# Kernel tuning notes

Hardware: AMD Instinct MI355X
Metric: run time of the kernel (lower is better)

Reference implementation:

```python
import jax, jax.numpy as jnp
import numpy as np

KEYS = ["A1", "B2", "E1", "E2", "E3", "E4", "E5"]
DIMS = [1, 1, 2, 2, 2, 2, 2]  # irrep dimensions for D12 point group
H = 8  # num_heads


def setup_inputs() -> dict:
    key = jax.random.key(0)
    ks = jax.random.split(key, 11)
    B, S, M = 8, 1024, 64  # batch, seq_len, multiplicity per key
    inp = {}
    for i, (name, d) in enumerate(zip(KEYS, DIMS)):
        inp[f"x_{name}"] = jax.random.normal(ks[i], (B, S, d, M), dtype=jnp.float32)
    for j, wn in enumerate(["Wq", "Wk", "Wv", "Wo"]):
        # per-key nn.Linear weights [out_mult, in_mult], stacked over the 7 keys
        inp[wn] = jax.random.normal(ks[7 + j], (7, M, M), dtype=jnp.float32) / np.float32(np.sqrt(M))
    return inp


def _split_heads(v):
    # [B,S,d,m] -> [B,H,S,d*mk]
    B, S, d, m = v.shape
    mk = m // H
    return v.reshape(B, S, d, H, mk).transpose(0, 3, 1, 2, 4).reshape(B, H, S, d * mk)


def _combine_heads(v, d):
    # [B,H,S,d*mk] -> [B,S,d,H*mk]
    B, _, S, dmk = v.shape
    mk = dmk // d
    return v.reshape(B, H, S, d, mk).transpose(0, 2, 3, 1, 4).reshape(B, S, d, H * mk)


def _forward(xs, Wq, Wk, Wv, Wo):
    # per-key bias-free linears on the multiplicity (last) axis; nn.Linear does x @ W.T
    qs = [_split_heads(jnp.einsum('bsdi,oi->bsdo', x, Wq[i])) for i, x in enumerate(xs)]
    kks = [_split_heads(jnp.einsum('bsdi,oi->bsdo', x, Wk[i])) for i, x in enumerate(xs)]
    vs = [_split_heads(jnp.einsum('bsdi,oi->bsdo', x, Wv[i])) for i, x in enumerate(xs)]
    Q = jnp.concatenate(qs, axis=-1)  # [B,H,S,D], D = sum d_k*mk = 96
    K = jnp.concatenate(kks, axis=-1)
    scale = np.float32(1.0 / np.sqrt(Q.shape[-1]))
    probs = jax.nn.softmax(jnp.einsum('bhqd,bhkd->bhqk', Q, K) * scale, axis=-1)
    outs = []
    for i, (v, d) in enumerate(zip(vs, DIMS)):
        o = jnp.einsum('bhqk,bhkd->bhqd', probs, v)  # shared softmax over per-key V branches
        o = _combine_heads(o, d)  # [B,S,d,M]
        outs.append(jnp.einsum('bsdi,oi->bsdo', o, Wo[i]))
    # concatenate the 7 per-key outputs along the irrep-dimension axis: [B,S,12,M]
    return jnp.concatenate(outs, axis=2)


def reference(x_A1, x_B2, x_E1, x_E2, x_E3, x_E4, x_E5, Wq, Wk, Wv, Wo):
    xs = [x_A1, x_B2, x_E1, x_E2, x_E3, x_E4, x_E5]
    return _forward(xs, Wq, Wk, Wv, Wo)
```

## Files before the change

### kernel.cpp

```cpp
#include <hip/hip_runtime.h>
#include <stdint.h>

typedef __attribute__((ext_vector_type(8))) short bf16x8;
typedef __attribute__((ext_vector_type(4))) float f32x4;
typedef unsigned short ushort_t;

__device__ __forceinline__ unsigned short f2bf(float f){
  union { float f; unsigned u; } c; c.f = f;
  unsigned u = c.u;
  u = u + 0x7FFFu + ((u >> 16) & 1u);
  return (unsigned short)(u >> 16);
}

__device__ __forceinline__ bf16x8 cvt8(const float* p){
  const float4 a = ((const float4*)p)[0];
  const float4 b = ((const float4*)p)[1];
  bf16x8 r;
  r[0]=(short)f2bf(a.x); r[1]=(short)f2bf(a.y); r[2]=(short)f2bf(a.z); r[3]=(short)f2bf(a.w);
  r[4]=(short)f2bf(b.x); r[5]=(short)f2bf(b.y); r[6]=(short)f2bf(b.z); r[7]=(short)f2bf(b.w);
  return r;
}

__device__ __forceinline__ uint32_t pk2bf(float a, float b){
  uint32_t r;
  asm("v_cvt_pk_bf16_f32 %0, %1, %2" : "=v"(r) : "v"(a), "v"(b));
  return r;
}

__device__ __forceinline__ float exp2x(float x){
  float r;
  asm("v_exp_f32 %0, %1" : "=v"(r) : "v"(x));
  return r;
}

__device__ __forceinline__ void gll16(const ushort_t* g, short* l){
  __builtin_amdgcn_global_load_lds(
      (const __attribute__((address_space(1))) unsigned int*)g,
      (__attribute__((address_space(3))) unsigned int*)l, 16, 0, 0);
}

__global__ __launch_bounds__(256) void wconv(
    const float* __restrict__ Wq, const float* __restrict__ Wk,
    const float* __restrict__ Wv, const float* __restrict__ Wo,
    ushort_t* __restrict__ out)
{
  const int a = blockIdx.y;
  const float* src = (a==0)?Wq:(a==1)?Wk:(a==2)?Wv:Wo;
  const float sc = (a==0) ? 0.14724743479535623f : 1.0f;
  const int i = (blockIdx.x*256 + threadIdx.x)*8;
  float4 v0 = *(const float4*)(src+i);
  float4 v1 = *(const float4*)(src+i+4);
  uint4 o;
  o.x = pk2bf(v0.x*sc, v0.y*sc);
  o.y = pk2bf(v0.z*sc, v0.w*sc);
  o.z = pk2bf(v1.x*sc, v1.y*sc);
  o.w = pk2bf(v1.z*sc, v1.w*sc);
  *(uint4*)(out + (size_t)a*28672 + i) = o;
}

__global__ __launch_bounds__(256) void qkv_proj(
    const float* __restrict__ xA1, const float* __restrict__ xB2,
    const float* __restrict__ xE1, const float* __restrict__ xE2,
    const float* __restrict__ xE3, const float* __restrict__ xE4,
    const float* __restrict__ xE5,
    const ushort_t* __restrict__ Wb4,
    ushort_t* __restrict__ Qg, ushort_t* __restrict__ Kg,
    ushort_t* __restrict__ Vg)
{
  const int dims[7] = {1,1,2,2,2,2,2};
  const int rrb_[7] = {0,1,2,4,6,8,10};
  const int tile = blockIdx.x;
  int i = 0, t0 = 0;
  for (int k = 0; k < 7; ++k){
    int n = 128 * dims[k];
    if (tile >= t0 + n) t0 += n; else { i = k; break; }
  }
  const int d = dims[i], rrb = rrb_[i];
  const float* xp = (i==0)?xA1:(i==1)?xB2:(i==2)?xE1:(i==3)?xE2:(i==4)?xE3:(i==5)?xE4:xE5;

  const int lane = threadIdx.x & 63;
  const int w    = threadIdx.x >> 6;
  const int lo = lane & 15, hi = lane >> 4;
  const int row0 = (tile - t0) * 64 + w * 16;

  bf16x8 afr[2];
  {
    const float* rp = xp + (size_t)(row0 + lo) * 64;
    afr[0] = cvt8(rp + 8*hi);
    afr[1] = cvt8(rp + 32 + 8*hi);
  }

  ushort_t* Ob[3] = {Qg, Kg, Vg};

  #pragma unroll
  for (int wsel = 0; wsel < 3; ++wsel){
    const ushort_t* Wb = Wb4 + (size_t)wsel*28672 + (size_t)i * 64 * 64;
    #pragma unroll
    for (int ot = 0; ot < 4; ++ot){
      f32x4 acc = {0.f,0.f,0.f,0.f};
      #pragma unroll
      for (int c = 0; c < 2; ++c){
        bf16x8 bfr = *(const bf16x8*)(Wb + (size_t)(lo + 16*ot) * 64 + 32*c + 8*hi);
        acc = __builtin_amdgcn_mfma_f32_16x16x32_bf16(afr[c], bfr, acc, 0, 0, 0);
      }
      const int o  = lo + 16*ot;
      const int hh = o >> 3, mm = o & 7;
      #pragma unroll
      for (int r = 0; r < 4; ++r){
        int R  = row0 + hi*4 + r;
        int bs = (d == 2) ? (R >> 1) : R;
        int dx = (d == 2) ? (R & 1)  : 0;
        int bb = bs >> 10, s = bs & 1023;
        int rr = rrb + dx;
        size_t tb = (size_t)((bb*8 + hh)*16 + (s >> 6)) * 6144;
        unsigned short val = f2bf(acc[r]);
        if (wsel < 2){
          size_t a = tb + (size_t)(((((s>>4)&3)*3 + (rr>>2))*64 + (rr&3)*16 + (s&15)))*8 + mm;
          Ob[wsel][a] = val;
        } else {
          int s6 = s & 63, rem = s6 & 31;
          int jj = (rem & 3) + ((rem >> 4) << 2);
          int f  = rr*8 + mm;
          size_t a = tb + (size_t)((((s6>>5)*6 + (f>>4))*64 + ((rem>>2)&3)*16 + (f&15)))*8 + jj;
          Ob[2][a] = val;
        }
      }
    }
  }
}

__global__ __launch_bounds__(256, 2) void attn(
    const ushort_t* __restrict__ Qg,
    const ushort_t* __restrict__ Kg,
    const ushort_t* __restrict__ Vg,
    ushort_t* __restrict__ Oc)
{
  __shared__ __align__(16) short Kl[2][6144];
  __shared__ __align__(16) short Vl[2][6144];

  const int bid = blockIdx.x;
  const int bh = (bid & 7)*8 + ((bid >> 3) & 7);
  const int qt = bid >> 6;
  const int b = bh >> 3, h = bh & 7;
  const int tid = threadIdx.x;
  const int w = tid >> 6, lane = tid & 63;
  const int lo = lane & 15, hi = lane >> 4;
  const size_t base = (size_t)bh * 16 * 6144;

  bf16x8 qf[2][3];
  #pragma unroll
  for (int g = 0; g < 2; ++g){
    int qq = qt*128 + w*32 + g*16;
    const ushort_t* qb = Qg + base + (size_t)(qq >> 6)*6144 + (size_t)(((qq>>4)&3)*3)*512;
    #pragma unroll
    for (int c = 0; c < 3; ++c)
      qf[g][c] = *(const bf16x8*)(qb + (c*64 + lane)*8);
  }

  f32x4 acc[6][2];
  #pragma unroll
  for (int ft = 0; ft < 6; ++ft){ acc[ft][0] = (f32x4){0,0,0,0}; acc[ft][1] = (f32x4){0,0,0,0}; }
  float mr[2] = {-1e30f, -1e30f}, lr[2] = {0.f, 0.f};

#define STAGE(tt, bb) do { \
    const ushort_t* kg_ = Kg + base + (size_t)(tt)*6144 + tid*8; \
    const ushort_t* vg_ = Vg + base + (size_t)(tt)*6144 + tid*8; \
    short* kl_ = &Kl[bb][tid*8]; short* vl_ = &Vl[bb][tid*8]; \
    gll16(kg_,        kl_);        gll16(kg_ + 2048, kl_ + 2048); \
    gll16(kg_ + 4096, kl_ + 4096); gll16(vg_,        vl_); \
    gll16(vg_ + 2048, vl_ + 2048); gll16(vg_ + 4096, vl_ + 4096); \
  } while(0)

  STAGE(0, 0);
  __syncthreads();

  for (int t = 0; t < 16; ++t){
    if (t < 15) STAGE(t+1, (t+1)&1);
    const int cb = t & 1;

    f32x4 st[2][4];
    #pragma unroll
    for (int kvb = 0; kvb < 4; ++kvb){
      bf16x8 kf[3];
      #pragma unroll
      for (int c = 0; c < 3; ++c)
        kf[c] = *(const bf16x8*)&Kl[cb][((kvb*3 + c)*64 + lane)*8];
      #pragma unroll
      for (int g = 0; g < 2; ++g){
        f32x4 s = {0.f,0.f,0.f,0.f};
        #pragma unroll
        for (int c = 0; c < 3; ++c)
          s = __builtin_amdgcn_mfma_f32_16x16x32_bf16(kf[c], qf[g][c], s, 0, 0, 0);
        st[g][kvb] = s;
      }
    }

    bf16x8 pb[2][2];
    #pragma unroll
    for (int g = 0; g < 2; ++g){
      float tm = st[g][0][0];
      #pragma unroll
      for (int kvb = 0; kvb < 4; ++kvb)
        #pragma unroll
        for (int r = 0; r < 4; ++r) tm = fmaxf(tm, st[g][kvb][r]);
      tm = fmaxf(tm, __shfl_xor(tm, 16));
      tm = fmaxf(tm, __shfl_xor(tm, 32));
      if (!__all(tm - mr[g] <= 8.f)){
        float mn = fmaxf(mr[g], tm);
        float al = exp2x(mr[g] - mn);
        lr[g] *= al;
        #pragma unroll
        for (int ft = 0; ft < 6; ++ft)
          #pragma unroll
          for (int r = 0; r < 4; ++r) acc[ft][g][r] *= al;
        mr[g] = mn;
      }
      float ps = 0.f;
      #pragma unroll
      for (int kvb = 0; kvb < 4; ++kvb)
        #pragma unroll
        for (int r = 0; r < 4; ++r){ st[g][kvb][r] = exp2x(st[g][kvb][r] - mr[g]); ps += st[g][kvb][r]; }
      ps += __shfl_xor(ps, 16);
      ps += __shfl_xor(ps, 32);
      lr[g] += ps;
      #pragma unroll
      for (int ch = 0; ch < 2; ++ch){
        union { uint32_t u[4]; bf16x8 v; } pu;
        pu.u[0] = pk2bf(st[g][2*ch  ][0], st[g][2*ch  ][1]);
        pu.u[1] = pk2bf(st[g][2*ch  ][2], st[g][2*ch  ][3]);
        pu.u[2] = pk2bf(st[g][2*ch+1][0], st[g][2*ch+1][1]);
        pu.u[3] = pk2bf(st[g][2*ch+1][2], st[g][2*ch+1][3]);
        pb[g][ch] = pu.v;
      }
    }

    #pragma unroll
    for (int ch = 0; ch < 2; ++ch){
      #pragma unroll
      for (int ft = 0; ft < 6; ++ft){
        bf16x8 va = *(const bf16x8*)&Vl[cb][((ch*6 + ft)*64 + lane)*8];
        acc[ft][0] = __builtin_amdgcn_mfma_f32_16x16x32_bf16(va, pb[0][ch], acc[ft][0], 0, 0, 0);
        acc[ft][1] = __builtin_amdgcn_mfma_f32_16x16x32_bf16(va, pb[1][ch], acc[ft][1], 0, 0, 0);
      }
    }

    __syncthreads();
  }
#undef STAGE

  #pragma unroll
  for (int g = 0; g < 2; ++g){
    float rl = 1.f / lr[g];
    int q = qt*128 + w*32 + g*16 + lo;
    #pragma unroll
    for (int ft = 0; ft < 6; ++ft){
      uint2 o;
      o.x = pk2bf(acc[ft][g][0]*rl, acc[ft][g][1]*rl);
      o.y = pk2bf(acc[ft][g][2]*rl, acc[ft][g][3]*rl);
      int f0 = ft*16 + 4*hi;
      int rr = f0 >> 3, mm0 = f0 & 7;
      size_t ad = ((size_t)(b*1024 + q)*12 + rr)*64 + h*8 + mm0;
      *(uint2*)(Oc + ad) = o;
    }
  }
}

__global__ __launch_bounds__(256) void out_proj(
    const ushort_t* __restrict__ Oc,
    const ushort_t* __restrict__ Wb4,
    float* __restrict__ out)
{
  const int dims[7] = {1,1,2,2,2,2,2};
  const int rrb_[7] = {0,1,2,4,6,8,10};
  const int tile = blockIdx.x;
  int i = 0, t0 = 0;
  for (int k = 0; k < 7; ++k){
    int n = 128 * dims[k];
    if (tile >= t0 + n) t0 += n; else { i = k; break; }
  }
  const int d = dims[i], rrb = rrb_[i];
  const int w = threadIdx.x >> 6, lane = threadIdx.x & 63;
  const int lo = lane & 15, hi = lane >> 4;
  const int row0 = (tile - t0) * 64 + w * 16;

  bf16x8 afr[2];
  {
    int R  = row0 + lo;
    int bs = (d == 2) ? (R >> 1) : R;
    int dx = (d == 2) ? (R & 1)  : 0;
    const ushort_t* rp = Oc + (size_t)(bs*12 + rrb + dx) * 64;
    afr[0] = *(const bf16x8*)(rp + 8*hi);
    afr[1] = *(const bf16x8*)(rp + 32 + 8*hi);
  }
  const ushort_t* Wb = Wb4 + (size_t)3*28672 + (size_t)i * 64 * 64;
  #pragma unroll
  for (int ot = 0; ot < 4; ++ot){
    f32x4 acc = {0.f,0.f,0.f,0.f};
    #pragma unroll
    for (int c = 0; c < 2; ++c){
      bf16x8 bfr = *(const bf16x8*)(Wb + (size_t)(lo + 16*ot) * 64 + 32*c + 8*hi);
      acc = __builtin_amdgcn_mfma_f32_16x16x32_bf16(afr[c], bfr, acc, 0, 0, 0);
    }
    #pragma unroll
    for (int r = 0; r < 4; ++r){
      int R  = row0 + hi*4 + r;
      int bs = (d == 2) ? (R >> 1) : R;
      int dx = (d == 2) ? (R & 1)  : 0;
      out[(size_t)(bs*12 + rrb + dx) * 64 + lo + 16*ot] = acc[r];
    }
  }
}

extern "C" void kernel_launch(void* const* d_in, const int* in_sizes, int n_in,
                              void* d_out, int out_size, void* d_ws, size_t ws_size,
                              hipStream_t stream)
{
  const float* xA1 = (const float*)d_in[0];
  const float* xB2 = (const float*)d_in[1];
  const float* xE1 = (const float*)d_in[2];
  const float* xE2 = (const float*)d_in[3];
  const float* xE3 = (const float*)d_in[4];
  const float* xE4 = (const float*)d_in[5];
  const float* xE5 = (const float*)d_in[6];
  const float* Wq  = (const float*)d_in[7];
  const float* Wk  = (const float*)d_in[8];
  const float* Wv  = (const float*)d_in[9];
  const float* Wo  = (const float*)d_in[10];

  const size_t NE = (size_t)8 * 1024 * 12 * 64;
  ushort_t* Qg = (ushort_t*)d_ws;
  ushort_t* Kg = Qg + NE;
  ushort_t* Vg = Kg + NE;
  ushort_t* Oc = Vg + NE;
  ushort_t* Wb4 = Oc + NE;

  wconv<<<dim3(14,4), dim3(256), 0, stream>>>(Wq, Wk, Wv, Wo, Wb4);
  qkv_proj<<<dim3(1536), dim3(256), 0, stream>>>(xA1,xB2,xE1,xE2,xE3,xE4,xE5,
                                                 Wb4, Qg,Kg,Vg);
  attn<<<dim3(512), dim3(256), 0, stream>>>(Qg,Kg,Vg, Oc);
  out_proj<<<dim3(1536), dim3(256), 0, stream>>>(Oc, Wb4, (float*)d_out);
}
```

Measured before the change: 81.95 us.

## Stage QKV stores through LDS, halve attention query tile, relayout Oc

qkv_proj now tiles by irrep row and writes each tile into shared memory first, then stores it to Q/K/V in 16-byte vectors instead of scattered 2-byte writes. The attention kernel handles 64 queries per block instead of 128 and launches twice as many blocks with a launch-bounds occupancy of 3. It also adds s_setprio around its MFMA phases. The attention output buffer gets a new head-major layout that out_proj reads with vector loads. The trade-off is more K/V reloads per query across blocks and extra LDS traffic plus barriers in the projection kernel.

```diff
diff --git a/kernel.cpp b/kernel.cpp
--- a/kernel.cpp
+++ b/kernel.cpp
@@ -37,6 +37,11 @@
   __builtin_amdgcn_global_load_lds(
       (const __attribute__((address_space(1))) unsigned int*)g,
       (__attribute__((address_space(3))) unsigned int*)l, 16, 0, 0);
+}
+
+__device__ __forceinline__ void rr_decode(int rr, int& i, int& dx, int& d){
+  if (rr < 2){ i = rr; dx = 0; d = 1; }
+  else { i = 2 + ((rr-2)>>1); dx = (rr-2)&1; d = 2; }
 }
 
 __global__ __launch_bounds__(256) void wconv(
@@ -67,25 +72,23 @@
     ushort_t* __restrict__ Qg, ushort_t* __restrict__ Kg,
     ushort_t* __restrict__ Vg)
 {
-  const int dims[7] = {1,1,2,2,2,2,2};
-  const int rrb_[7] = {0,1,2,4,6,8,10};
+  __shared__ short Cl[64*72];
+
   const int tile = blockIdx.x;
-  int i = 0, t0 = 0;
-  for (int k = 0; k < 7; ++k){
-    int n = 128 * dims[k];
-    if (tile >= t0 + n) t0 += n; else { i = k; break; }
-  }
-  const int d = dims[i], rrb = rrb_[i];
+  const int rr = tile >> 7, rt = tile & 127;
+  int i, dx, d; rr_decode(rr, i, dx, d);
   const float* xp = (i==0)?xA1:(i==1)?xB2:(i==2)?xE1:(i==3)?xE2:(i==4)?xE3:(i==5)?xE4:xE5;
 
   const int lane = threadIdx.x & 63;
   const int w    = threadIdx.x >> 6;
   const int lo = lane & 15, hi = lane >> 4;
-  const int row0 = (tile - t0) * 64 + w * 16;
+  const int b8 = (rt >> 4) * 8;
+  const int tile64 = rt & 15;
 
   bf16x8 afr[2];
   {
-    const float* rp = xp + (size_t)(row0 + lo) * 64;
+    const int R = rt*64 + w*16 + lo;
+    const float* rp = xp + (size_t)(R*d + dx) * 64;
     afr[0] = cvt8(rp + 8*hi);
     afr[1] = cvt8(rp + 32 + 8*hi);
   }
@@ -94,7 +97,7 @@
 
   #pragma unroll
   for (int wsel = 0; wsel < 3; ++wsel){
-    const ushort_t* Wb = Wb4 + (size_t)wsel*28672 + (size_t)i * 64 * 64;
+    const ushort_t* Wb = Wb4 + (size_t)wsel*28672 + (size_t)i * 4096;
     #pragma unroll
     for (int ot = 0; ot < 4; ++ot){
       f32x4 acc = {0.f,0.f,0.f,0.f};
@@ -103,33 +106,45 @@
         bf16x8 bfr = *(const bf16x8*)(Wb + (size_t)(lo + 16*ot) * 64 + 32*c + 8*hi);
         acc = __builtin_amdgcn_mfma_f32_16x16x32_bf16(afr[c], bfr, acc, 0, 0, 0);
       }
-      const int o  = lo + 16*ot;
-      const int hh = o >> 3, mm = o & 7;
-      #pragma unroll
-      for (int r = 0; r < 4; ++r){
-        int R  = row0 + hi*4 + r;
-        int bs = (d == 2) ? (R >> 1) : R;
-        int dx = (d == 2) ? (R & 1)  : 0;
-        int bb = bs >> 10, s = bs & 1023;
-        int rr = rrb + dx;
-        size_t tb = (size_t)((bb*8 + hh)*16 + (s >> 6)) * 6144;
-        unsigned short val = f2bf(acc[r]);
-        if (wsel < 2){
-          size_t a = tb + (size_t)(((((s>>4)&3)*3 + (rr>>2))*64 + (rr&3)*16 + (s&15)))*8 + mm;
-          Ob[wsel][a] = val;
-        } else {
-          int s6 = s & 63, rem = s6 & 31;
-          int jj = (rem & 3) + ((rem >> 4) << 2);
-          int f  = rr*8 + mm;
-          size_t a = tb + (size_t)((((s6>>5)*6 + (f>>4))*64 + ((rem>>2)&3)*16 + (f&15)))*8 + jj;
-          Ob[2][a] = val;
+      #pragma unroll
+      for (int r = 0; r < 4; ++r)
+        Cl[(w*16 + hi*4 + r)*72 + lo + 16*ot] = (short)f2bf(acc[r]);
+    }
+    __syncthreads();
+
+    if (wsel < 2){
+      #pragma unroll
+      for (int cc = 0; cc < 2; ++cc){
+        int c2 = threadIdx.x + cc*256;
+        int sl = c2 & 63, hh = c2 >> 6;
+        bf16x8 v = *(const bf16x8*)&Cl[sl*72 + hh*8];
+        size_t a = (size_t)((b8 + hh)*16 + tile64)*6144
+                 + (size_t)(((sl>>4)*3 + (rr>>2))*64 + (rr&3)*16 + (sl&15))*8;
+        *(bf16x8*)(Ob[wsel] + a) = v;
+      }
+    } else {
+      #pragma unroll
+      for (int cc = 0; cc < 2; ++cc){
+        int c2 = threadIdx.x + cc*256;
+        int mm = c2 & 7, hh = (c2>>3)&7, sblk = c2>>6;
+        int a5 = sblk>>2, slot = sblk&3;
+        short tmp[8];
+        #pragma unroll
+        for (int jj = 0; jj < 8; ++jj){
+          int s_j = a5*32 + (jj>>2)*16 + slot*4 + (jj&3);
+          tmp[jj] = Cl[s_j*72 + hh*8 + mm];
         }
-      }
-    }
-  }
-}
-
-__global__ __launch_bounds__(256, 2) void attn(
+        int fh = rr>>1, fl = (rr&1)*8 + mm;
+        size_t a = (size_t)((b8 + hh)*16 + tile64)*6144
+                 + (size_t)((a5*6 + fh)*64 + slot*16 + fl)*8;
+        *(bf16x8*)(Vg + a) = *(const bf16x8*)tmp;
+      }
+    }
+    __syncthreads();
+  }
+}
+
+__global__ __launch_bounds__(256, 3) void attn(
     const ushort_t* __restrict__ Qg,
     const ushort_t* __restrict__ Kg,
     const ushort_t* __restrict__ Vg,
@@ -141,26 +156,23 @@
   const int bid = blockIdx.x;
   const int bh = (bid & 7)*8 + ((bid >> 3) & 7);
   const int qt = bid >> 6;
-  const int b = bh >> 3, h = bh & 7;
   const int tid = threadIdx.x;
   const int w = tid >> 6, lane = tid & 63;
   const int lo = lane & 15, hi = lane >> 4;
   const size_t base = (size_t)bh * 16 * 6144;
 
-  bf16x8 qf[2][3];
+  bf16x8 qf[3];
+  {
+    const ushort_t* qb = Qg + base + (size_t)qt*6144 + (size_t)(w*3)*512;
+    #pragma unroll
+    for (int c = 0; c < 3; ++c)
+      qf[c] = *(const bf16x8*)(qb + (c*64 + lane)*8);
+  }
+
+  f32x4 acc[6];
   #pragma unroll
-  for (int g = 0; g < 2; ++g){
-    int qq = qt*128 + w*32 + g*16;
-    const ushort_t* qb = Qg + base + (size_t)(qq >> 6)*6144 + (size_t)(((qq>>4)&3)*3)*512;
-    #pragma unroll
-    for (int c = 0; c < 3; ++c)
-      qf[g][c] = *(const bf16x8*)(qb + (c*64 + lane)*8);
-  }
-
-  f32x4 acc[6][2];
-  #pragma unroll
-  for (int ft = 0; ft < 6; ++ft){ acc[ft][0] = (f32x4){0,0,0,0}; acc[ft][1] = (f32x4){0,0,0,0}; }
-  float mr[2] = {-1e30f, -1e30f}, lr[2] = {0.f, 0.f};
+  for (int ft = 0; ft < 6; ++ft) acc[ft] = (f32x4){0,0,0,0};
+  float mr = -1e30f, lr = 0.f;
 
 #define STAGE(tt, bb) do { \
     const ushort_t* kg_ = Kg + base + (size_t)(tt)*6144 + tid*8; \
@@ -178,88 +190,81 @@
     if (t < 15) STAGE(t+1, (t+1)&1);
     const int cb = t & 1;
 
-    f32x4 st[2][4];
+    f32x4 st[4];
+    __builtin_amdgcn_s_setprio(1);
     #pragma unroll
     for (int kvb = 0; kvb < 4; ++kvb){
-      bf16x8 kf[3];
-      #pragma unroll
-      for (int c = 0; c < 3; ++c)
-        kf[c] = *(const bf16x8*)&Kl[cb][((kvb*3 + c)*64 + lane)*8];
-      #pragma unroll
-      for (int g = 0; g < 2; ++g){
-        f32x4 s = {0.f,0.f,0.f,0.f};
+      f32x4 s = {0.f,0.f,0.f,0.f};
+      #pragma unroll
+      for (int c = 0; c < 3; ++c){
+        bf16x8 kf = *(const bf16x8*)&Kl[cb][((kvb*3 + c)*64 + lane)*8];
+        s = __builtin_amdgcn_mfma_f32_16x16x32_bf16(kf, qf[c], s, 0, 0, 0);
+      }
+      st[kvb] = s;
+    }
+    __builtin_amdgcn_s_setprio(0);
+
+    float tm = st[0][0];
+    #pragma unroll
+    for (int kvb = 0; kvb < 4; ++kvb)
+      #pragma unroll
+      for (int r = 0; r < 4; ++r) tm = fmaxf(tm, st[kvb][r]);
+    tm = fmaxf(tm, __shfl_xor(tm, 16));
+    tm = fmaxf(tm, __shfl_xor(tm, 32));
+    if (!__all(tm - mr <= 8.f)){
+      float mn = fmaxf(mr, tm);
+      float al = exp2x(mr - mn);
+      lr *= al;
+      #pragma unroll
+      for (int ft = 0; ft < 6; ++ft)
         #pragma unroll
-        for (int c = 0; c < 3; ++c)
-          s = __builtin_amdgcn_mfma_f32_16x16x32_bf16(kf[c], qf[g][c], s, 0, 0, 0);
-        st[g][kvb] = s;
-      }
-    }
-
-    bf16x8 pb[2][2];
-    #pragma unroll
-    for (int g = 0; g < 2; ++g){
-      float tm = st[g][0][0];
-      #pragma unroll
-      for (int kvb = 0; kvb < 4; ++kvb)
-        #pragma unroll
-        for (int r = 0; r < 4; ++r) tm = fmaxf(tm, st[g][kvb][r]);
-      tm = fmaxf(tm, __shfl_xor(tm, 16));
-      tm = fmaxf(tm, __shfl_xor(tm, 32));
-      if (!__all(tm - mr[g] <= 8.f)){
-        float mn = fmaxf(mr[g], tm);
-        float al = exp2x(mr[g] - mn);
-        lr[g] *= al;
-        #pragma unroll
-        for (int ft = 0; ft < 6; ++ft)
-          #pragma unroll
-          for (int r = 0; r < 4; ++r) acc[ft][g][r] *= al;
-        mr[g] = mn;
-      }
-      float ps = 0.f;
-      #pragma unroll
-      for (int kvb = 0; kvb < 4; ++kvb)
-        #pragma unroll
-        for (int r = 0; r < 4; ++r){ st[g][kvb][r] = exp2x(st[g][kvb][r] - mr[g]); ps += st[g][kvb][r]; }
-      ps += __shfl_xor(ps, 16);
-      ps += __shfl_xor(ps, 32);
-      lr[g] += ps;
-      #pragma unroll
-      for (int ch = 0; ch < 2; ++ch){
-        union { uint32_t u[4]; bf16x8 v; } pu;
-        pu.u[0] = pk2bf(st[g][2*ch  ][0], st[g][2*ch  ][1]);
-        pu.u[1] = pk2bf(st[g][2*ch  ][2], st[g][2*ch  ][3]);
-        pu.u[2] = pk2bf(st[g][2*ch+1][0], st[g][2*ch+1][1]);
-        pu.u[3] = pk2bf(st[g][2*ch+1][2], st[g][2*ch+1][3]);
-        pb[g][ch] = pu.v;
-      }
-    }
-
+        for (int r = 0; r < 4; ++r) acc[ft][r] *= al;
+      mr = mn;
+    }
+    float ps = 0.f;
+    #pragma unroll
+    for (int kvb = 0; kvb < 4; ++kvb)
+      #pragma unroll
+      for (int r = 0; r < 4; ++r){ st[kvb][r] = exp2x(st[kvb][r] - mr); ps += st[kvb][r]; }
+    ps += __shfl_xor(ps, 16);
+    ps += __shfl_xor(ps, 32);
+    lr += ps;
+
+    bf16x8 pb[2];
+    #pragma unroll
+    for (int ch = 0; ch < 2; ++ch){
+      union { uint32_t u[4]; bf16x8 v; } pu;
+      pu.u[0] = pk2bf(st[2*ch  ][0], st[2*ch  ][1]);
+      pu.u[1] = pk2bf(st[2*ch  ][2], st[2*ch  ][3]);
+      pu.u[2] = pk2bf(st[2*ch+1][0], st[2*ch+1][1]);
+      pu.u[3] = pk2bf(st[2*ch+1][2], st[2*ch+1][3]);
+      pb[ch] = pu.v;
+    }
+
+    __builtin_amdgcn_s_setprio(1);
     #pragma unroll
     for (int ch = 0; ch < 2; ++ch){
       #pragma unroll
       for (int ft = 0; ft < 6; ++ft){
         bf16x8 va = *(const bf16x8*)&Vl[cb][((ch*6 + ft)*64 + lane)*8];
-        acc[ft][0] = __builtin_amdgcn_mfma_f32_16x16x32_bf16(va, pb[0][ch], acc[ft][0], 0, 0, 0);
-        acc[ft][1] = __builtin_amdgcn_mfma_f32_16x16x32_bf16(va, pb[1][ch], acc[ft][1], 0, 0, 0);
-      }
-    }
+        acc[ft] = __builtin_amdgcn_mfma_f32_16x16x32_bf16(va, pb[ch], acc[ft], 0, 0, 0);
+      }
+    }
+    __builtin_amdgcn_s_setprio(0);
 
     __syncthreads();
   }
 #undef STAGE
 
-  #pragma unroll
-  for (int g = 0; g < 2; ++g){
-    float rl = 1.f / lr[g];
-    int q = qt*128 + w*32 + g*16 + lo;
+  {
+    float rl = 1.f / lr;
+    int q = qt*64 + w*16 + lo;
     #pragma unroll
     for (int ft = 0; ft < 6; ++ft){
       uint2 o;
-      o.x = pk2bf(acc[ft][g][0]*rl, acc[ft][g][1]*rl);
-      o.y = pk2bf(acc[ft][g][2]*rl, acc[ft][g][3]*rl);
-      int f0 = ft*16 + 4*hi;
-      int rr = f0 >> 3, mm0 = f0 & 7;
-      size_t ad = ((size_t)(b*1024 + q)*12 + rr)*64 + h*8 + mm0;
+      o.x = pk2bf(acc[ft][0]*rl, acc[ft][1]*rl);
+      o.y = pk2bf(acc[ft][2]*rl, acc[ft][3]*rl);
+      size_t ad = ((size_t)(bh*24 + ft*4 + hi)*1024 + q)*4;
       *(uint2*)(Oc + ad) = o;
     }
   }
@@ -270,29 +275,29 @@
     const ushort_t* __restrict__ Wb4,
     float* __restrict__ out)
 {
-  const int dims[7] = {1,1,2,2,2,2,2};
-  const int rrb_[7] = {0,1,2,4,6,8,10};
   const int tile = blockIdx.x;
-  int i = 0, t0 = 0;
-  for (int k = 0; k < 7; ++k){
-    int n = 128 * dims[k];
-    if (tile >= t0 + n) t0 += n; else { i = k; break; }
-  }
-  const int d = dims[i], rrb = rrb_[i];
-  const int w = threadIdx.x >> 6, lane = threadIdx.x & 63;
+  const int rr = tile >> 7, rt = tile & 127;
+  int i, dx, d; rr_decode(rr, i, dx, d); (void)dx; (void)d;
+
+  const int lane = threadIdx.x & 63;
+  const int w    = threadIdx.x >> 6;
   const int lo = lane & 15, hi = lane >> 4;
-  const int row0 = (tile - t0) * 64 + w * 16;
 
   bf16x8 afr[2];
   {
-    int R  = row0 + lo;
-    int bs = (d == 2) ? (R >> 1) : R;
-    int dx = (d == 2) ? (R & 1)  : 0;
-    const ushort_t* rp = Oc + (size_t)(bs*12 + rrb + dx) * 64;
-    afr[0] = *(const bf16x8*)(rp + 8*hi);
-    afr[1] = *(const bf16x8*)(rp + 32 + 8*hi);
-  }
-  const ushort_t* Wb = Wb4 + (size_t)3*28672 + (size_t)i * 64 * 64;
+    const int R = rt*64 + w*16 + lo;
+    const int b = R >> 10, s = R & 1023;
+    union { uint2 u2[2]; bf16x8 v; } a0, a1;
+    #pragma unroll
+    for (int jj = 0; jj < 2; ++jj){
+      a0.u2[jj] = *(const uint2*)(Oc + ((size_t)((b*8 + hi)*24 + 2*rr + jj)*1024 + s)*4);
+      a1.u2[jj] = *(const uint2*)(Oc + ((size_t)((b*8 + 4 + hi)*24 + 2*rr + jj)*1024 + s)*4);
+    }
+    afr[0] = a0.v;
+    afr[1] = a1.v;
+  }
+
+  const ushort_t* Wb = Wb4 + (size_t)3*28672 + (size_t)i * 4096;
   #pragma unroll
   for (int ot = 0; ot < 4; ++ot){
     f32x4 acc = {0.f,0.f,0.f,0.f};
@@ -303,10 +308,8 @@
     }
     #pragma unroll
     for (int r = 0; r < 4; ++r){
-      int R  = row0 + hi*4 + r;
-      int bs = (d == 2) ? (R >> 1) : R;
-      int dx = (d == 2) ? (R & 1)  : 0;
-      out[(size_t)(bs*12 + rrb + dx) * 64 + lo + 16*ot] = acc[r];
+      int bs = rt*64 + w*16 + hi*4 + r;
+      out[(size_t)(bs*12 + rr)*64 + lo + 16*ot] = acc[r];
     }
   }
 }
@@ -337,6 +340,6 @@
   wconv<<<dim3(14,4), dim3(256), 0, stream>>>(Wq, Wk, Wv, Wo, Wb4);
   qkv_proj<<<dim3(1536), dim3(256), 0, stream>>>(xA1,xB2,xE1,xE2,xE3,xE4,xE5,
                                                  Wb4, Qg,Kg,Vg);
-  attn<<<dim3(512), dim3(256), 0, stream>>>(Qg,Kg,Vg, Oc);
+  attn<<<dim3(1024), dim3(256), 0, stream>>>(Qg,Kg,Vg, Oc);
   out_proj<<<dim3(1536), dim3(256), 0, stream>>>(Oc, Wb4, (float*)d_out);
 }
```

After: 90.62 us. 1.11x slower.
